# Performance work log

Measured on AMD Instinct MI355X. Metric: run time of the kernel, lower is better.

## Reference

```python
import jax, jax.numpy as jnp
import numpy as np

B, N, D = 8, 1024, 512
H, DH = 8, 64          # num_heads, dim_head_output
MLP = 2048
PRUNE_NUM = 64         # remove_num > 0 -> prune branch of determine_fuse
KEEP_NUM = 3
NEG = -1e10


def setup_inputs() -> dict:
    key = jax.random.key(0)
    ks = jax.random.split(key, 10)
    s = 0.02
    inp = {
        "x": jax.random.normal(ks[0], (B, N, D), dtype=jnp.float32),
        "mask": (jax.random.uniform(ks[1], (B, N, N)) < 0.1).astype(jnp.float32),
        "Wqkv": jax.random.normal(ks[2], (D, 3 * H * DH), dtype=jnp.float32) * s,
        "Wout": jax.random.normal(ks[3], (H * DH, D), dtype=jnp.float32) * s,
        "bout": jnp.zeros((D,), jnp.float32),
        "ln1_g": jnp.ones((D,), jnp.float32),
        "ln1_b": jnp.zeros((D,), jnp.float32),
        "ln2_g": jnp.ones((D,), jnp.float32),
        "ln2_b": jnp.zeros((D,), jnp.float32),
        "W1": jax.random.normal(ks[4], (D, MLP), dtype=jnp.float32) * s,
        "b1": jnp.zeros((MLP,), jnp.float32),
        "W2": jax.random.normal(ks[5], (MLP, D), dtype=jnp.float32) * s,
        "b2": jnp.zeros((D,), jnp.float32),
    }
    return inp


def _layer_norm(x, g, b, eps=1e-5):
    mu = jnp.mean(x, axis=-1, keepdims=True)
    var = jnp.mean((x - mu) ** 2, axis=-1, keepdims=True)
    return (x - mu) * jax.lax.rsqrt(var + eps) * g + b


def _attention_with_gos(h, mask, Wqkv, Wout, bout):
    # qkv projection (no bias), chunk into q,k,v then b n (h d) -> b h n d
    qkv = h @ Wqkv                                  # [B,N,3*H*DH]
    q, k, v = jnp.split(qkv, 3, axis=-1)
    def heads(t):
        return t.reshape(B, N, H, DH).transpose(0, 2, 1, 3)  # bhnd
    q, k, v = heads(q), heads(k), heads(v)
    scale = DH ** -0.5
    scores = jnp.einsum("bhnd,bhmd->bhnm", q, k) * scale
    scores = jnp.where(mask[:, None, :, :] == 1.0, NEG, scores)
    attw = jax.nn.softmax(scores, axis=-1)          # [B,H,N,N]
    out = jnp.einsum("bhnm,bhmd->bhnd", attw, v)
    out = out.transpose(0, 2, 1, 3).reshape(B, N, H * DH)
    out = out @ Wout + bout                         # [B,N,D] (dropout=0 -> identity)

    # att_weights_topk = attw.mean(heads)[:, 0]; [:,0] = -inf
    att_topk = attw.mean(axis=1)[:, 0]              # [B,N]
    att_topk = att_topk.at[:, 0].set(-jnp.inf)

    # determine_fuse (prune branch, remove_num > 0)
    nrm = jnp.linalg.norm(out, axis=2, keepdims=True)
    normed = out / jnp.maximum(nrm, 1e-12)          # F.normalize(p=2, dim=2)
    cos = jnp.einsum("bnd,bmd->bnm", normed, normed)
    idx = jnp.arange(N)
    cos = cos.at[:, idx, idx].set(-jnp.inf)
    cos = cos.at[:, 0, :].set(-jnp.inf)
    cos = cos.at[:, :, 0].set(-jnp.inf)
    # NOTE: torch also computes topk of cos.view(B,-1) with k=(N-1)^2, but the
    # result is unused in the remove_num>0 branch (dead code under jit).

    # torch.topk(att_topk, N) sorted descending -> argsort of -att_topk
    attentive_idx = jnp.argsort(-att_topk, axis=1)  # [B,N]
    # pruned = attentive_idx[:, :N-1][:, -PRUNE_NUM:]
    what_to_prune = attentive_idx[:, N - 1 - PRUNE_NUM : N - 1]
    what_to_merge = jnp.full((B, 1), -1, dtype=jnp.int32)
    survived_mask = jnp.zeros((B, 1 + KEEP_NUM, 1 + KEEP_NUM), dtype=jnp.int32)
    return out, what_to_prune, what_to_merge, survived_mask


def reference(x, mask, Wqkv, Wout, bout, ln1_g, ln1_b, ln2_g, ln2_b, W1, b1, W2, b2):
    h = _layer_norm(x, ln1_g, ln1_b)
    att_out, what_to_prune, what_to_merge, survived_mask = _attention_with_gos(
        h, mask, Wqkv, Wout, bout)
    x = x + att_out
    h2 = _layer_norm(x, ln2_g, ln2_b)
    ff = jax.nn.gelu(h2 @ W1 + b1, approximate=False) @ W2 + b2
    x = x + ff
    return x, what_to_prune, what_to_merge, survived_mask
```

## Files before the change

kernel.cpp:

```cpp
#include <hip/hip_runtime.h>
#include <hip/hip_bf16.h>
#include <math.h>

#define BB 8
#define NN 1024
#define DD 512
#define HH 8
#define DHH 64
#define MLPD 2048

typedef __attribute__((ext_vector_type(8))) short short8;
typedef __attribute__((ext_vector_type(4))) float f32x4;

#define MFMA16(a,b,c) __builtin_amdgcn_mfma_f32_16x16x32_bf16(a,b,c,0,0,0)

#define QSCALE 0.18033688011112042f
#define NEGBIG 0xCE6E6B28u

__device__ __forceinline__ short f2bf(float f) {
  union { float f; unsigned u; } x; x.f = f;
  unsigned r = x.u + 0x7FFFu + ((x.u >> 16) & 1u);
  return (short)(r >> 16);
}

__device__ __forceinline__ void gl_lds16(const short* g, short* l) {
  __builtin_amdgcn_global_load_lds(
      (const __attribute__((address_space(1))) unsigned int*)g,
      (__attribute__((address_space(3))) unsigned int*)l, 16, 0, 0);
}

__device__ __forceinline__ float gelu_fast(float t) {
  const float u = 0.7978845608028654f * (t + 0.044715f * t * t * t);
  const float e = __builtin_amdgcn_exp2f(u * 2.8853900817779268f);
  return t - t * __builtin_amdgcn_rcpf(e + 1.0f);
}

template<bool WF32>
__global__ __launch_bounds__(256) void ln_kernel(const float* __restrict__ x,
    const float* __restrict__ gam, const float* __restrict__ bet,
    short* __restrict__ ob, float* __restrict__ of)
{
  const int row = blockIdx.x;
  const int tid = threadIdx.x;
  const float2 xv = *(const float2*)(x + (size_t)row*DD + tid*2);
  double s = (double)xv.x + (double)xv.y;
  for (int o = 32; o >= 1; o >>= 1) s += __shfl_down(s, o, 64);
  __shared__ double red[4];
  const int l = tid & 63, w = tid >> 6;
  if (l == 0) red[w] = s;
  __syncthreads();
  const double mu = (red[0]+red[1]+red[2]+red[3]) * (1.0/512.0);
  const double d0 = (double)xv.x - mu, d1 = (double)xv.y - mu;
  double q = d0*d0 + d1*d1;
  for (int o = 32; o >= 1; o >>= 1) q += __shfl_down(q, o, 64);
  __syncthreads();
  if (l == 0) red[w] = q;
  __syncthreads();
  const double var = (red[0]+red[1]+red[2]+red[3]) * (1.0/512.0);
  const float rs = (float)(1.0 / sqrt(var + 1e-5));
  const float mf = (float)mu;
  const float y0 = (xv.x - mf)*rs*gam[tid*2]   + bet[tid*2];
  const float y1 = (xv.y - mf)*rs*gam[tid*2+1] + bet[tid*2+1];
  ob[(size_t)row*DD + tid*2]   = f2bf(y0);
  ob[(size_t)row*DD + tid*2+1] = f2bf(y1);
  if (WF32) {
    of[(size_t)row*DD + tid*2]   = y0;
    of[(size_t)row*DD + tid*2+1] = y1;
  }
}

__global__ __launch_bounds__(256) void wtall_kernel(
    const float* __restrict__ Wqkv, const float* __restrict__ Wout,
    const float* __restrict__ W1,   const float* __restrict__ W2,
    short* __restrict__ Wqkvt, short* __restrict__ Woutt,
    short* __restrict__ W1t,   short* __restrict__ W2t)
{
  const int id = blockIdx.x;
  const float* W; short* Wt; int K, N, t;
  if (id < 768)       { W = Wqkv; Wt = Wqkvt; K = 512;  N = 1536; t = id; }
  else if (id < 1024) { W = Wout; Wt = Woutt; K = 512;  N = 512;  t = id - 768; }
  else if (id < 2048) { W = W1;   Wt = W1t;   K = 512;  N = 2048; t = id - 1024; }
  else                { W = W2;   Wt = W2t;   K = 2048; N = 512;  t = id - 2048; }
  const int nx = N >> 5;
  const int n0 = (t % nx)*32, k0 = (t / nx)*32;
  __shared__ float tile[32][33];
  const int tx = threadIdx.x & 31, ty = threadIdx.x >> 5;
  #pragma unroll
  for (int j = 0; j < 4; j++)
    tile[ty + j*8][tx] = W[(size_t)(k0 + ty + j*8)*N + n0 + tx];
  __syncthreads();
  #pragma unroll
  for (int j = 0; j < 4; j++)
    Wt[(size_t)(n0 + ty + j*8)*K + k0 + tx] = f2bf(tile[tx][ty + j*8]);
}

__global__ __launch_bounds__(256) void maskpack_kernel(const float* __restrict__ mask,
    unsigned long long* __restrict__ mb)
{
  const int wid = blockIdx.x*256 + threadIdx.x;
  if (wid >= BB*NN*16) return;
  const int r = wid >> 4, c = wid & 15;
  const float4* p = (const float4*)(mask + (size_t)r*NN + c*64);
  unsigned long long m = 0;
  #pragma unroll
  for (int i = 0; i < 16; i++) {
    const float4 v = p[i];
    unsigned long long mm = 0;
    if (v.x == 1.0f) mm |= 1ULL;
    if (v.y == 1.0f) mm |= 2ULL;
    if (v.z == 1.0f) mm |= 4ULL;
    if (v.w == 1.0f) mm |= 8ULL;
    m |= mm << (i*4);
  }
  mb[wid] = m;
}

template<int BN, int EPI, int NBUF>
__global__ __launch_bounds__(256) void gemm_bt(
    const short* __restrict__ A, const short* __restrict__ Bt,
    int M, int N, int K,
    const float* __restrict__ bias, const float* __restrict__ res,
    float* __restrict__ outf, short* __restrict__ outb,
    short* __restrict__ outQ, short* __restrict__ outK, short* __restrict__ outVt)
{
  constexpr int CH = 8 + BN/16;
  constexpr int L  = CH/4;
  constexpr int BUFS = (128 + BN)*32;
  __shared__ __align__(16) short lds[NBUF*BUFS];
  const int tid = threadIdx.x;
  const int bm0 = blockIdx.x * 128;
  const int bn0 = blockIdx.y * BN;
  const int lane = tid & 63, wid = tid >> 6;
  const int wm = (wid >> 1) * 64, wn = (wid & 1) * (BN/2);
  const int lr = lane & 15, lg = lane >> 4;
  constexpr int NT = BN/32;

  const short* gsrc[L];
  int loff[L];
  const int scc = (((lane & 3) ^ ((lane >> 3) & 3)))*8;
  #pragma unroll
  for (int i = 0; i < L; i++) {
    const int c = i*4 + wid;
    const int rr = ((c < 8) ? c : c - 8)*16 + (lane >> 2);
    gsrc[i] = (c < 8) ? (A + (size_t)(bm0 + rr)*K + scc)
                      : (Bt + (size_t)(bn0 + rr)*K + scc);
    loff[i] = c*512;
  }
  const int xs = (lr >> 1) & 3;

  f32x4 acc[4][NT];
  #pragma unroll
  for (int i = 0; i < 4; i++)
    #pragma unroll
    for (int j = 0; j < NT; j++) acc[i][j] = f32x4{0.f,0.f,0.f,0.f};

  const int nsteps = K >> 5;

  auto STAGE = [&](int buf, int t) {
    short* dst = lds + buf*BUFS;
    const int ko = t*32;
    #pragma unroll
    for (int i = 0; i < L; i++)
      gl_lds16(gsrc[i] + ko, dst + loff[i]);
  };
  auto COMPUTE = [&](const short* bufA) {
    const short* bufB = bufA + 4096;
    short8 af[4], bfr[NT];
    #pragma unroll
    for (int mt = 0; mt < 4; mt++)
      af[mt] = *(const short8*)(bufA + (wm + mt*16 + lr)*32 + (lg ^ xs)*8);
    #pragma unroll
    for (int nt = 0; nt < NT; nt++)
      bfr[nt] = *(const short8*)(bufB + (wn + nt*16 + lr)*32 + (lg ^ xs)*8);
    __builtin_amdgcn_s_setprio(1);
    #pragma unroll
    for (int mt = 0; mt < 4; mt++)
      #pragma unroll
      for (int nt = 0; nt < NT; nt++)
        acc[mt][nt] = MFMA16(af[mt], bfr[nt], acc[mt][nt]);
    __builtin_amdgcn_s_setprio(0);
  };

  if constexpr (NBUF == 2) {
    STAGE(0, 0);
    asm volatile("s_waitcnt vmcnt(0)" ::: "memory");
    __builtin_amdgcn_s_barrier();
    int cur = 0;
    #pragma unroll 1
    for (int t = 0; t < nsteps; t++) {
      if (t + 1 < nsteps) STAGE(cur ^ 1, t + 1);
      COMPUTE(lds + cur*BUFS);
      asm volatile("s_waitcnt vmcnt(0)" ::: "memory");
      __builtin_amdgcn_s_barrier();
      cur ^= 1;
    }
  } else {
    STAGE(0, 0);
    STAGE(1, 1);
    int cur = 0;
    #pragma unroll 1
    for (int t = 0; t < nsteps; t++) {
      if (t == nsteps - 1) {
        asm volatile("s_waitcnt vmcnt(0)" ::: "memory");
      } else if constexpr (L == 4) {
        asm volatile("s_waitcnt vmcnt(4)" ::: "memory");
      } else {
        asm volatile("s_waitcnt vmcnt(3)" ::: "memory");
      }
      __builtin_amdgcn_s_barrier();
      if (t + 2 < nsteps) {
        const int bnext = (cur == 0) ? 2 : cur - 1;
        STAGE(bnext, t + 2);
      }
      COMPUTE(lds + cur*BUFS);
      cur = (cur == 2) ? 0 : cur + 1;
    }
  }

  if (EPI == 0 && bn0 >= 1024) {
    #pragma unroll
    for (int mt = 0; mt < 4; mt++)
      #pragma unroll
      for (int nt = 0; nt < NT; nt++) {
        const int row0 = bm0 + wm + mt*16 + lg*4;
        const int b = row0 >> 10, tok0 = row0 & 1023;
        const int c2 = bn0 + wn + nt*16 + lr - 1024;
        const int h = c2 >> 6, d = c2 & 63;
        unsigned lo2, hi2;
        asm("v_cvt_pk_bf16_f32 %0, %1, %2" : "=v"(lo2)
            : "v"(acc[mt][nt][0]), "v"(acc[mt][nt][1]));
        asm("v_cvt_pk_bf16_f32 %0, %1, %2" : "=v"(hi2)
            : "v"(acc[mt][nt][2]), "v"(acc[mt][nt][3]));
        uint2 pw; pw.x = lo2; pw.y = hi2;
        *(uint2*)(outVt + (((size_t)(b*HH + h))*DHH + d)*NN + tok0) = pw;
      }
    return;
  }

  #pragma unroll
  for (int mt = 0; mt < 4; mt++)
    #pragma unroll
    for (int nt = 0; nt < NT; nt++)
      #pragma unroll
      for (int r = 0; r < 4; r++) {
        const int row = bm0 + wm + mt*16 + lg*4 + r;
        const int col = bn0 + wn + nt*16 + lr;
        const float v = acc[mt][nt][r];
        if (EPI == 0) {
          const int b = row >> 10, tok = row & 1023;
          if (col < 512) {
            const int h = col >> 6, d = col & 63;
            outQ[(((size_t)(b*HH + h))*NN + tok)*DHH + d] = f2bf(v * QSCALE);
          } else {
            const int c2 = col - 512, h = c2 >> 6, d = c2 & 63;
            outK[(((size_t)(b*HH + h))*NN + tok)*DHH + d] = f2bf(v);
          }
        } else if (EPI == 1) {
          outf[(size_t)row*N + col] = v + bias[col] + res[(size_t)row*N + col];
        } else {
          outb[(size_t)row*N + col] = f2bf(gelu_fast(v + bias[col]));
        }
      }
}

__global__ __launch_bounds__(256) void attn_kernel(
    const short* __restrict__ Qg, const short* __restrict__ Kg,
    const short* __restrict__ Vtg, const unsigned long long* __restrict__ mb,
    short* __restrict__ attout)
{
  const int id = blockIdx.x;
  const int bh = (id & 7)*8 + ((id >> 3) & 7);
  const int qb = id >> 6;
  const int b = bh >> 3, h = bh & 7;
  const int tid = threadIdx.x, lane = tid & 63, w = tid >> 6;
  const int lr = lane & 15, lg = lane >> 4;

  __shared__ __align__(16) short K0[64*64], K1[64*64];
  __shared__ __align__(16) short V0[64*64], V1[64*64];
  __shared__ __align__(16) short PsA[4][16*72], PsB[4][16*72];

  const int qA = qb*128 + w*32 + lr;
  const int qB = qA + 16;
  short* PsAw = &PsA[w][0];
  short* PsBw = &PsB[w][0];

  const size_t qbase = (size_t)bh*NN*DHH;
  const short8 bqA0 = *(const short8*)(Qg + qbase + (size_t)qA*DHH + lg*8);
  const short8 bqA1 = *(const short8*)(Qg + qbase + (size_t)qA*DHH + 32 + lg*8);
  const short8 bqB0 = *(const short8*)(Qg + qbase + (size_t)qB*DHH + lg*8);
  const short8 bqB1 = *(const short8*)(Qg + qbase + (size_t)qB*DHH + 32 + lg*8);

  const unsigned long long* mrowA = mb + ((size_t)b*NN + qA)*16;
  const unsigned long long* mrowB = mb + ((size_t)b*NN + qB)*16;

  const int l8 = lane >> 3;
  const int uu = (lane & 7) ^ l8;
  const short* kgA = Kg + ((size_t)bh*NN + w*16 + l8)*64 + uu*8;
  const short* kgB = kgA + 8*64;
  const short* vgA = Vtg + ((size_t)bh*DHH + w*16 + l8)*NN + uu*8;
  const short* vgB = vgA + 8*NN;
  auto STAGE = [&](short* kb, short* vb, int kc) {
    gl_lds16(kgA + kc*4096, kb + (w*16)*64);
    gl_lds16(kgB + kc*4096, kb + (w*16 + 8)*64);
    gl_lds16(vgA + kc*64,   vb + (w*16)*64);
    gl_lds16(vgB + kc*64,   vb + (w*16 + 8)*64);
  };
  const int xo0 = ((lg ^ (lr & 7)))*8;
  const int xo1 = (((lg ^ (lr & 7))) ^ 4)*8;

  unsigned long long mAc, mBc, mAn, mBn;

  STAGE(K0, V0, 0);
  mAc = mrowA[0]; mBc = mrowB[0];
  asm volatile("s_waitcnt vmcnt(0)" ::: "memory");
  __builtin_amdgcn_s_barrier();

  f32x4 oA[4], oB[4];
  #pragma unroll
  for (int dt = 0; dt < 4; dt++) { oA[dt] = f32x4{0.f,0.f,0.f,0.f}; oB[dt] = f32x4{0.f,0.f,0.f,0.f}; }
  float lsumA = 0.f, lsumB = 0.f;

#define ATT_BODY(CK, CV, NK, NV, MAc, MBc, MAn, MBn, KC, LAST)                 \
  {                                                                            \
    if (!(LAST)) {                                                             \
      STAGE(NK, NV, (KC)+1);                                                   \
      MAn = mrowA[(KC)+1]; MBn = mrowB[(KC)+1];                                \
    }                                                                          \
                              \
    f32x4 sA[4], sB[4];                                                        \
    {                                                                          \
      const unsigned long long mqA = MAc >> (lg*4);                            \
      const unsigned loA = (unsigned)mqA, hiA = (unsigned)(mqA >> 32);         \
      const unsigned long long mqB = MBc >> (lg*4);                            \
      const unsigned loB = (unsigned)mqB, hiB = (unsigned)(mqB >> 32);         \
      _Pragma("unroll")                                                        \
      for (int nt = 0; nt < 4; nt++) {                                         \
        const unsigned wA = (nt < 2) ? loA : hiA;                              \
        const unsigned wB = (nt < 2) ? loB : hiB;                              \
        const int sh = (nt & 1) * 16;                                          \
        _Pragma("unroll")                                                      \
        for (int rr = 0; rr < 4; rr++) {                                       \
          const unsigned bA = (wA >> (sh + rr)) & 1u;                          \
          const unsigned bB = (wB >> (sh + rr)) & 1u;                          \
          sA[nt][rr] = __uint_as_float((0u - bA) & NEGBIG);                    \
          sB[nt][rr] = __uint_as_float((0u - bB) & NEGBIG);                    \
        }                                                                      \
      }                                                                        \
    }                                                                          \
    __builtin_amdgcn_s_setprio(1);                                             \
    _Pragma("unroll")                                                          \
    for (int nt = 0; nt < 4; nt++) {                                           \
      const short* kr = (CK) + (nt*16 + lr)*64;                                \
      const short8 ak0 = *(const short8*)(kr + xo0);                           \
      const short8 ak1 = *(const short8*)(kr + xo1);                           \
      sA[nt] = MFMA16(ak0, bqA0, sA[nt]);                                      \
      sA[nt] = MFMA16(ak1, bqA1, sA[nt]);                                      \
      sB[nt] = MFMA16(ak0, bqB0, sB[nt]);                                      \
      sB[nt] = MFMA16(ak1, bqB1, sB[nt]);                                      \
    }                                                                          \
    __builtin_amdgcn_s_setprio(0);                                             \
    _Pragma("unroll")                                                          \
    for (int nt = 0; nt < 4; nt++) {                                           \
      const float a0 = __builtin_amdgcn_exp2f(sA[nt][0]);                      \
      const float a1 = __builtin_amdgcn_exp2f(sA[nt][1]);                      \
      const float a2 = __builtin_amdgcn_exp2f(sA[nt][2]);                      \
      const float a3 = __builtin_amdgcn_exp2f(sA[nt][3]);                      \
      lsumA += (a0 + a1) + (a2 + a3);                                          \
      unsigned plo, phi;                                                       \
      asm("v_cvt_pk_bf16_f32 %0, %1, %2" : "=v"(plo) : "v"(a0), "v"(a1));      \
      asm("v_cvt_pk_bf16_f32 %0, %1, %2" : "=v"(phi) : "v"(a2), "v"(a3));      \
      uint2 pw; pw.x = plo; pw.y = phi;                                        \
      *(uint2*)(PsAw + lr*72 + nt*16 + lg*4) = pw;                             \
      const float c0 = __builtin_amdgcn_exp2f(sB[nt][0]);                      \
      const float c1 = __builtin_amdgcn_exp2f(sB[nt][1]);                      \
      const float c2 = __builtin_amdgcn_exp2f(sB[nt][2]);                      \
      const float c3 = __builtin_amdgcn_exp2f(sB[nt][3]);                      \
      lsumB += (c0 + c1) + (c2 + c3);                                          \
      unsigned qlo, qhi;                                                       \
      asm("v_cvt_pk_bf16_f32 %0, %1, %2" : "=v"(qlo) : "v"(c0), "v"(c1));      \
      asm("v_cvt_pk_bf16_f32 %0, %1, %2" : "=v"(qhi) : "v"(c2), "v"(c3));      \
      uint2 qw; qw.x = qlo; qw.y = qhi;                                        \
      *(uint2*)(PsBw + lr*72 + nt*16 + lg*4) = qw;                             \
    }                                                                          \
    {                                                                          \
      const short8 bpA0 = *(const short8*)(PsAw + lr*72 + lg*8);               \
      const short8 bpA1 = *(const short8*)(PsAw + lr*72 + 32 + lg*8);          \
      const short8 bpB0 = *(const short8*)(PsBw + lr*72 + lg*8);               \
      const short8 bpB1 = *(const short8*)(PsBw + lr*72 + 32 + lg*8);          \
      __builtin_amdgcn_s_setprio(1);                                           \
      _Pragma("unroll")                                                        \
      for (int dt = 0; dt < 4; dt++) {                                         \
        const short* vr = (CV) + (dt*16 + lr)*64;                              \
        const short8 av0 = *(const short8*)(vr + xo0);                         \
        const short8 av1 = *(const short8*)(vr + xo1);                         \
        oA[dt] = MFMA16(av0, bpA0, oA[dt]);                                    \
        oA[dt] = MFMA16(av1, bpA1, oA[dt]);                                    \
        oB[dt] = MFMA16(av0, bpB0, oB[dt]);                                    \
        oB[dt] = MFMA16(av1, bpB1, oB[dt]);                                    \
      }                                                                        \
      __builtin_amdgcn_s_setprio(0);                                           \
    }                                                                          \
    if (!(LAST)) {                                                             \
      asm volatile("s_waitcnt vmcnt(0)" ::: "memory");                         \
      __builtin_amdgcn_s_barrier();                                            \
      MAc = MAn; MBc = MBn;                                                    \
    }                                                                          \
  }

  #pragma unroll 1
  for (int kc = 0; kc < 16; kc += 2) {
    ATT_BODY(K0, V0, K1, V1, mAc, mBc, mAn, mBn, kc, false)
    ATT_BODY(K1, V1, K0, V0, mAc, mBc, mAn, mBn, kc+1, (kc+1) == 15)
  }
#undef ATT_BODY

  lsumA += __shfl_xor(lsumA, 16, 64);
  lsumA += __shfl_xor(lsumA, 32, 64);
  lsumB += __shfl_xor(lsumB, 16, 64);
  lsumB += __shfl_xor(lsumB, 32, 64);
  const float linvA = 1.0f / lsumA;
  const float linvB = 1.0f / lsumB;

  #pragma unroll
  for (int dt = 0; dt < 4; dt++) {
    unsigned w0, w1, w2, w3;
    const float a0 = oA[dt][0]*linvA, a1 = oA[dt][1]*linvA;
    const float a2 = oA[dt][2]*linvA, a3 = oA[dt][3]*linvA;
    asm("v_cvt_pk_bf16_f32 %0, %1, %2" : "=v"(w0) : "v"(a0), "v"(a1));
    asm("v_cvt_pk_bf16_f32 %0, %1, %2" : "=v"(w1) : "v"(a2), "v"(a3));
    uint2 ow; ow.x = w0; ow.y = w1;
    *(uint2*)(PsAw + lr*72 + dt*16 + lg*4) = ow;
    const float c0 = oB[dt][0]*linvB, c1 = oB[dt][1]*linvB;
    const float c2 = oB[dt][2]*linvB, c3 = oB[dt][3]*linvB;
    asm("v_cvt_pk_bf16_f32 %0, %1, %2" : "=v"(w2) : "v"(c0), "v"(c1));
    asm("v_cvt_pk_bf16_f32 %0, %1, %2" : "=v"(w3) : "v"(c2), "v"(c3));
    uint2 ow2; ow2.x = w2; ow2.y = w3;
    *(uint2*)(PsBw + lr*72 + dt*16 + lg*4) = ow2;
  }
  #pragma unroll
  for (int rep = 0; rep < 2; rep++) {
    const int c = lane + rep*64;
    const int row = c >> 3, off = c & 7;
    const uint4 ovA = *(const uint4*)(PsAw + row*72 + off*8);
    *(uint4*)(attout + ((size_t)b*NN + qb*128 + w*32 + row)*DD + h*DHH + off*8) = ovA;
    const uint4 ovB = *(const uint4*)(PsBw + row*72 + off*8);
    *(uint4*)(attout + ((size_t)b*NN + qb*128 + w*32 + 16 + row)*DD + h*DHH + off*8) = ovB;
  }
}

__global__ __launch_bounds__(512) void q0wv_kernel(const float* __restrict__ hlnf,
    const float* __restrict__ Wqkv, double* __restrict__ wv)
{
  const int bh = blockIdx.x, b = bh >> 3, h = bh & 7;
  __shared__ double red[512];
  __shared__ double q0s[64];
  {
    const int d = threadIdx.x & 63, cg = threadIdx.x >> 6;
    double acc = 0.0;
    #pragma unroll 8
    for (int c = cg*64; c < cg*64 + 64; c++)
      acc += (double)hlnf[(size_t)b*NN*DD + c] * (double)Wqkv[(size_t)c*1536 + h*64 + d];
    red[threadIdx.x] = acc;
    __syncthreads();
    if (threadIdx.x < 64) {
      double s = 0.0;
      #pragma unroll
      for (int g = 0; g < 8; g++) s += red[g*64 + d];
      q0s[d] = s;
    }
    __syncthreads();
  }
  const int c = threadIdx.x;
  const float4* wp = (const float4*)(Wqkv + (size_t)c*1536 + 512 + h*64);
  double acc = 0.0;
  #pragma unroll
  for (int dv = 0; dv < 16; dv++) {
    const float4 wq = wp[dv];
    acc += q0s[dv*4+0]*(double)wq.x + q0s[dv*4+1]*(double)wq.y
         + q0s[dv*4+2]*(double)wq.z + q0s[dv*4+3]*(double)wq.w;
  }
  wv[(size_t)bh*512 + c] = acc;
}

__global__ __launch_bounds__(256) void srow_kernel(const float* __restrict__ hlnf,
    const double* __restrict__ wv, const float* __restrict__ mask,
    double* __restrict__ srow)
{
  const int b = blockIdx.x, jc = blockIdx.y;
  const int jl = threadIdx.x >> 3;
  const int cg = threadIdx.x & 7;
  const int j  = jc*32 + jl;
  __shared__ double lw[8*512];
  __shared__ double red[32][8][9];
  for (int i = threadIdx.x; i < 4096; i += 256) lw[i] = wv[(size_t)b*4096 + i];
  __syncthreads();
  double acc[8] = {0,0,0,0,0,0,0,0};
  const float* xr = hlnf + ((size_t)b*NN + j)*DD;
  #pragma unroll
  for (int i = 0; i < 16; i++) {
    const int c = cg*4 + i*32;
    const float4 xv4 = *(const float4*)(xr + c);
    #pragma unroll
    for (int h = 0; h < 8; h++) {
      const double* lwc = lw + h*512 + c;
      acc[h] += (double)xv4.x*lwc[0] + (double)xv4.y*lwc[1]
              + (double)xv4.z*lwc[2] + (double)xv4.w*lwc[3];
    }
  }
  #pragma unroll
  for (int h = 0; h < 8; h++) red[jl][cg][h] = acc[h];
  __syncthreads();
  const int j2 = threadIdx.x >> 3, h2 = threadIdx.x & 7;
  double s = 0.0;
  #pragma unroll
  for (int g = 0; g < 8; g++) s += red[j2][g][h2];
  s *= 0.125;
  const float mval = mask[(size_t)b*NN*NN + jc*32 + j2];
  if (mval == 1.0f) s = -1e10;
  srow[((size_t)b*8 + h2)*NN + jc*32 + j2] = s;
}

__global__ __launch_bounds__(1024) void sumatt_kernel(const double* __restrict__ srow,
    double* __restrict__ attv)
{
  const int b = blockIdx.x;
  const int t = threadIdx.x;
  __shared__ double e[8][1024];
  __shared__ double red[1024];
  __shared__ double sinv[8];
  const int h = t >> 7, j0 = t & 127;
  double ps = 0.0;
  #pragma unroll
  for (int i = 0; i < 8; i++) {
    const int j = j0 + i*128;
    const double v = exp(srow[((size_t)b*8 + h)*NN + j]);
    e[h][j] = v;
    ps += v;
  }
  red[t] = ps;
  __syncthreads();
  #pragma unroll
  for (int off = 64; off >= 1; off >>= 1) {
    if (j0 < off) red[t] += red[t + off];
    __syncthreads();
  }
  if (j0 == 0) sinv[h] = 1.0 / red[t];
  __syncthreads();
  double s = 0.0;
  #pragma unroll
  for (int hh = 0; hh < 8; hh++) s += e[hh][t] * sinv[hh];
  attv[b*NN + t] = (t == 0) ? -INFINITY : s * 0.125;
}

__global__ __launch_bounds__(256) void rank_kernel(const double* __restrict__ attv,
    float* __restrict__ dout, int offP, int offM, int offS)
{
  const int b = blockIdx.x, jc = blockIdx.y;
  const int t = threadIdx.x;
  __shared__ double a[1024];
  __shared__ int red[32][8];
  #pragma unroll
  for (int rep = 0; rep < 4; rep++)
    a[rep*256 + t] = attv[b*NN + rep*256 + t];
  __syncthreads();
  const int jl = t >> 3, kg = t & 7;
  const int j = jc*32 + jl;
  const double aj = a[j];
  int r = 0;
  #pragma unroll 8
  for (int i = 0; i < 128; i++) {
    const int idx = kg*128 + ((i + kg*2) & 127);
    const double ak = a[idx];
    r += ((ak > aj) || (ak == aj && idx < j)) ? 1 : 0;
  }
  red[jl][kg] = r;
  __syncthreads();
  if (t < 32) {
    int rr = 0;
    #pragma unroll
    for (int g = 0; g < 8; g++) rr += red[t][g];
    const int jj = jc*32 + t;
    if (rr >= 959 && rr <= 1022) dout[offP + b*64 + (rr - 959)] = (float)jj;
  }
  if (b == 0 && jc == 0) {
    if (t < 8)   dout[offM + t] = -1.0f;
    if (t < 128) dout[offS + t] = 0.0f;
  }
}

extern "C" void kernel_launch(void* const* d_in, const int* in_sizes, int n_in,
                              void* d_out, int out_size, void* d_ws, size_t ws_size,
                              hipStream_t stream) {
  (void)in_sizes; (void)n_in; (void)out_size; (void)ws_size;
  const float* x     = (const float*)d_in[0];
  const float* mask  = (const float*)d_in[1];
  const float* Wqkv  = (const float*)d_in[2];
  const float* Wout  = (const float*)d_in[3];
  const float* bout  = (const float*)d_in[4];
  const float* ln1g  = (const float*)d_in[5];
  const float* ln1b  = (const float*)d_in[6];
  const float* ln2g  = (const float*)d_in[7];
  const float* ln2b  = (const float*)d_in[8];
  const float* W1    = (const float*)d_in[9];
  const float* b1    = (const float*)d_in[10];
  const float* W2    = (const float*)d_in[11];
  const float* b2    = (const float*)d_in[12];
  float* dout = (float*)d_out;

  const size_t MB = 1ull << 20;
  char* ws = (char*)d_ws;
  short*  hln_bf = (short*)(ws + 0);
  float*  hlnf   = (float*)(ws + 8*MB);
  short*  Qg     = (short*)(ws + 24*MB);
  short*  Kg     = (short*)(ws + 32*MB);
  short*  Vtg    = (short*)(ws + 40*MB);
  unsigned long long* mbits = (unsigned long long*)(ws + 48*MB);
  short*  Wqkvt  = (short*)(ws + 49*MB);
  short*  Woutt  = (short*)(ws + 51*MB);
  short*  W1t    = (short*)(ws + 52*MB);
  short*  W2t    = (short*)(ws + 54*MB);
  double* wvv    = (double*)(ws + 56*MB + 256*1024);
  double* srow   = (double*)(ws + 57*MB);
  double* attv   = (double*)(ws + 59*MB);
  short*  attout = (short*)(ws + 60*MB);
  float*  x1     = (float*)(ws + 68*MB);
  short*  h2     = (short*)(ws + 84*MB);
  short*  gbuf   = (short*)(ws + 0);

  const int offP = BB*NN*DD;
  const int offM = offP + BB*64;
  const int offS = offM + BB;

  ln_kernel<true><<<BB*NN, 256, 0, stream>>>(x, ln1g, ln1b, hln_bf, hlnf);

  q0wv_kernel<<<BB*HH, 512, 0, stream>>>(hlnf, Wqkv, wvv);
  srow_kernel<<<dim3(BB, 32), 256, 0, stream>>>(hlnf, wvv, mask, srow);
  sumatt_kernel<<<BB, 1024, 0, stream>>>(srow, attv);
  rank_kernel<<<dim3(BB, 32), 256, 0, stream>>>(attv, dout, offP, offM, offS);

  maskpack_kernel<<<(BB*NN*16)/256, 256, 0, stream>>>(mask, mbits);
  wtall_kernel<<<3072, 256, 0, stream>>>(Wqkv, Wout, W1, W2,
      Wqkvt, Woutt, W1t, W2t);

  gemm_bt<128,0,3><<<dim3(64, 12), 256, 0, stream>>>(hln_bf, Wqkvt, BB*NN, 1536, 512,
      nullptr, nullptr, nullptr, nullptr, Qg, Kg, Vtg);

  attn_kernel<<<512, 256, 0, stream>>>(Qg, Kg, Vtg, mbits, attout);

  gemm_bt<64,1,3><<<dim3(64, 8), 256, 0, stream>>>(attout, Woutt, BB*NN, 512, 512,
      bout, x, x1, nullptr, nullptr, nullptr, nullptr);

  ln_kernel<false><<<BB*NN, 256, 0, stream>>>(x1, ln2g, ln2b, h2, nullptr);

  gemm_bt<64,2,3><<<dim3(64, 32), 256, 0, stream>>>(h2, W1t, BB*NN, 2048, 512,
      b1, nullptr, nullptr, gbuf, nullptr, nullptr, nullptr);

  gemm_bt<64,1,3><<<dim3(64, 8), 256, 0, stream>>>(gbuf, W2t, BB*NN, 512, 2048,
      b2, x1, dout, nullptr, nullptr, nullptr, nullptr);
}
```

Before: 196.4 us.

## Fuse prep kernels, store residual in bf16, widen FFN1 GEMM tile

Merges the first layer norm, mask bit-packing and weight transpose/convert into a single prep kernel to cut launch count. The post-attention residual is stored as bf16 instead of fp32, with a new epilogue mode that writes bf16 and another that reads the bf16 residual for the final add. The second layer norm reads this bf16 buffer. The FFN1 GEMM switches to a 128-wide N tile with double buffering. The bf16 residual reduces memory traffic but loses precision in the skip connection.

Measured after the change: 189.1 us. 3.7% less time.

```diff
diff --git a/kernel.cpp b/kernel.cpp
--- a/kernel.cpp
+++ b/kernel.cpp
@@ -22,6 +22,11 @@
   unsigned r = x.u + 0x7FFFu + ((x.u >> 16) & 1u);
   return (short)(r >> 16);
 }
+__device__ __forceinline__ float bf2f(short s) {
+  union { float f; unsigned u; } x;
+  x.u = ((unsigned)(unsigned short)s) << 16;
+  return x.f;
+}
 
 __device__ __forceinline__ void gl_lds16(const short* g, short* l) {
   __builtin_amdgcn_global_load_lds(
@@ -35,22 +40,96 @@
   return t - t * __builtin_amdgcn_rcpf(e + 1.0f);
 }
 
-template<bool WF32>
-__global__ __launch_bounds__(256) void ln_kernel(const float* __restrict__ x,
+__global__ __launch_bounds__(256) void prep_kernel(
+    const float* __restrict__ x, const float* __restrict__ ln1g,
+    const float* __restrict__ ln1b, short* __restrict__ hln_bf,
+    float* __restrict__ hlnf,
+    const float* __restrict__ mask, unsigned long long* __restrict__ mbits,
+    const float* __restrict__ Wqkv, const float* __restrict__ Wout,
+    const float* __restrict__ W1,   const float* __restrict__ W2,
+    short* __restrict__ Wqkvt, short* __restrict__ Woutt,
+    short* __restrict__ W1t,   short* __restrict__ W2t)
+{
+  const int id = blockIdx.x;
+  const int tid = threadIdx.x;
+  if (id < 8192) {
+    __shared__ double red[4];
+    const int row = id;
+    const float2 xv = *(const float2*)(x + (size_t)row*DD + tid*2);
+    double s = (double)xv.x + (double)xv.y;
+    for (int o = 32; o >= 1; o >>= 1) s += __shfl_down(s, o, 64);
+    const int l = tid & 63, w = tid >> 6;
+    if (l == 0) red[w] = s;
+    __syncthreads();
+    const double mu = (red[0]+red[1]+red[2]+red[3]) * (1.0/512.0);
+    const double d0 = (double)xv.x - mu, d1 = (double)xv.y - mu;
+    double q = d0*d0 + d1*d1;
+    for (int o = 32; o >= 1; o >>= 1) q += __shfl_down(q, o, 64);
+    __syncthreads();
+    if (l == 0) red[w] = q;
+    __syncthreads();
+    const double var = (red[0]+red[1]+red[2]+red[3]) * (1.0/512.0);
+    const float rs = (float)(1.0 / sqrt(var + 1e-5));
+    const float mf = (float)mu;
+    const float y0 = (xv.x - mf)*rs*ln1g[tid*2]   + ln1b[tid*2];
+    const float y1 = (xv.y - mf)*rs*ln1g[tid*2+1] + ln1b[tid*2+1];
+    hln_bf[(size_t)row*DD + tid*2]   = f2bf(y0);
+    hln_bf[(size_t)row*DD + tid*2+1] = f2bf(y1);
+    hlnf[(size_t)row*DD + tid*2]   = y0;
+    hlnf[(size_t)row*DD + tid*2+1] = y1;
+  } else if (id < 8704) {
+    const int wid = (id - 8192)*256 + tid;
+    const int r = wid >> 4, c = wid & 15;
+    const float4* p = (const float4*)(mask + (size_t)r*NN + c*64);
+    unsigned long long m = 0;
+    #pragma unroll
+    for (int i = 0; i < 16; i++) {
+      const float4 v = p[i];
+      unsigned long long mm = 0;
+      if (v.x == 1.0f) mm |= 1ULL;
+      if (v.y == 1.0f) mm |= 2ULL;
+      if (v.z == 1.0f) mm |= 4ULL;
+      if (v.w == 1.0f) mm |= 8ULL;
+      m |= mm << (i*4);
+    }
+    mbits[wid] = m;
+  } else {
+    const int id2 = id - 8704;
+    const float* W; short* Wt; int K, N, t;
+    if (id2 < 768)       { W = Wqkv; Wt = Wqkvt; K = 512;  N = 1536; t = id2; }
+    else if (id2 < 1024) { W = Wout; Wt = Woutt; K = 512;  N = 512;  t = id2 - 768; }
+    else if (id2 < 2048) { W = W1;   Wt = W1t;   K = 512;  N = 2048; t = id2 - 1024; }
+    else                 { W = W2;   Wt = W2t;   K = 2048; N = 512;  t = id2 - 2048; }
+    const int nx = N >> 5;
+    const int n0 = (t % nx)*32, k0 = (t / nx)*32;
+    __shared__ float tile[32][33];
+    const int tx = tid & 31, ty = tid >> 5;
+    #pragma unroll
+    for (int j = 0; j < 4; j++)
+      tile[ty + j*8][tx] = W[(size_t)(k0 + ty + j*8)*N + n0 + tx];
+    __syncthreads();
+    #pragma unroll
+    for (int j = 0; j < 4; j++)
+      Wt[(size_t)(n0 + ty + j*8)*K + k0 + tx] = f2bf(tile[tx][ty + j*8]);
+  }
+}
+
+__global__ __launch_bounds__(256) void ln2_kernel(const short* __restrict__ xb,
     const float* __restrict__ gam, const float* __restrict__ bet,
-    short* __restrict__ ob, float* __restrict__ of)
+    short* __restrict__ ob)
 {
   const int row = blockIdx.x;
   const int tid = threadIdx.x;
-  const float2 xv = *(const float2*)(x + (size_t)row*DD + tid*2);
-  double s = (double)xv.x + (double)xv.y;
+  const short2 xs = *(const short2*)(xb + (size_t)row*DD + tid*2);
+  const float x0 = bf2f(xs.x), x1v = bf2f(xs.y);
+  double s = (double)x0 + (double)x1v;
   for (int o = 32; o >= 1; o >>= 1) s += __shfl_down(s, o, 64);
   __shared__ double red[4];
   const int l = tid & 63, w = tid >> 6;
   if (l == 0) red[w] = s;
   __syncthreads();
   const double mu = (red[0]+red[1]+red[2]+red[3]) * (1.0/512.0);
-  const double d0 = (double)xv.x - mu, d1 = (double)xv.y - mu;
+  const double d0 = (double)x0 - mu, d1 = (double)x1v - mu;
   double q = d0*d0 + d1*d1;
   for (int o = 32; o >= 1; o >>= 1) q += __shfl_down(q, o, 64);
   __syncthreads();
@@ -59,60 +138,8 @@
   const double var = (red[0]+red[1]+red[2]+red[3]) * (1.0/512.0);
   const float rs = (float)(1.0 / sqrt(var + 1e-5));
   const float mf = (float)mu;
-  const float y0 = (xv.x - mf)*rs*gam[tid*2]   + bet[tid*2];
-  const float y1 = (xv.y - mf)*rs*gam[tid*2+1] + bet[tid*2+1];
-  ob[(size_t)row*DD + tid*2]   = f2bf(y0);
-  ob[(size_t)row*DD + tid*2+1] = f2bf(y1);
-  if (WF32) {
-    of[(size_t)row*DD + tid*2]   = y0;
-    of[(size_t)row*DD + tid*2+1] = y1;
-  }
-}
-
-__global__ __launch_bounds__(256) void wtall_kernel(
-    const float* __restrict__ Wqkv, const float* __restrict__ Wout,
-    const float* __restrict__ W1,   const float* __restrict__ W2,
-    short* __restrict__ Wqkvt, short* __restrict__ Woutt,
-    short* __restrict__ W1t,   short* __restrict__ W2t)
-{
-  const int id = blockIdx.x;
-  const float* W; short* Wt; int K, N, t;
-  if (id < 768)       { W = Wqkv; Wt = Wqkvt; K = 512;  N = 1536; t = id; }
-  else if (id < 1024) { W = Wout; Wt = Woutt; K = 512;  N = 512;  t = id - 768; }
-  else if (id < 2048) { W = W1;   Wt = W1t;   K = 512;  N = 2048; t = id - 1024; }
-  else                { W = W2;   Wt = W2t;   K = 2048; N = 512;  t = id - 2048; }
-  const int nx = N >> 5;
-  const int n0 = (t % nx)*32, k0 = (t / nx)*32;
-  __shared__ float tile[32][33];
-  const int tx = threadIdx.x & 31, ty = threadIdx.x >> 5;
-  #pragma unroll
-  for (int j = 0; j < 4; j++)
-    tile[ty + j*8][tx] = W[(size_t)(k0 + ty + j*8)*N + n0 + tx];
-  __syncthreads();
-  #pragma unroll
-  for (int j = 0; j < 4; j++)
-    Wt[(size_t)(n0 + ty + j*8)*K + k0 + tx] = f2bf(tile[tx][ty + j*8]);
-}
-
-__global__ __launch_bounds__(256) void maskpack_kernel(const float* __restrict__ mask,
-    unsigned long long* __restrict__ mb)
-{
-  const int wid = blockIdx.x*256 + threadIdx.x;
-  if (wid >= BB*NN*16) return;
-  const int r = wid >> 4, c = wid & 15;
-  const float4* p = (const float4*)(mask + (size_t)r*NN + c*64);
-  unsigned long long m = 0;
-  #pragma unroll
-  for (int i = 0; i < 16; i++) {
-    const float4 v = p[i];
-    unsigned long long mm = 0;
-    if (v.x == 1.0f) mm |= 1ULL;
-    if (v.y == 1.0f) mm |= 2ULL;
-    if (v.z == 1.0f) mm |= 4ULL;
-    if (v.w == 1.0f) mm |= 8ULL;
-    m |= mm << (i*4);
-  }
-  mb[wid] = m;
+  ob[(size_t)row*DD + tid*2]   = f2bf((x0  - mf)*rs*gam[tid*2]   + bet[tid*2]);
+  ob[(size_t)row*DD + tid*2+1] = f2bf((x1v - mf)*rs*gam[tid*2+1] + bet[tid*2+1]);
 }
 
 template<int BN, int EPI, int NBUF>
@@ -120,6 +147,7 @@
     const short* __restrict__ A, const short* __restrict__ Bt,
     int M, int N, int K,
     const float* __restrict__ bias, const float* __restrict__ res,
+    const short* __restrict__ resb,
     float* __restrict__ outf, short* __restrict__ outb,
     short* __restrict__ outQ, short* __restrict__ outK, short* __restrict__ outVt)
 {
@@ -255,10 +283,12 @@
             const int c2 = col - 512, h = c2 >> 6, d = c2 & 63;
             outK[(((size_t)(b*HH + h))*NN + tok)*DHH + d] = f2bf(v);
           }
-        } else if (EPI == 1) {
-          outf[(size_t)row*N + col] = v + bias[col] + res[(size_t)row*N + col];
+        } else if (EPI == 2) {
+          outb[(size_t)row*N + col] = f2bf(gelu_fast(v + bias[col]));
+        } else if (EPI == 3) {
+          outb[(size_t)row*N + col] = f2bf(v + bias[col] + res[(size_t)row*N + col]);
         } else {
-          outb[(size_t)row*N + col] = f2bf(gelu_fast(v + bias[col]));
+          outf[(size_t)row*N + col] = v + bias[col] + bf2f(resb[(size_t)row*N + col]);
         }
       }
 }
@@ -326,7 +356,6 @@
       STAGE(NK, NV, (KC)+1);                                                   \
       MAn = mrowA[(KC)+1]; MBn = mrowB[(KC)+1];                                \
     }                                                                          \
-                              \
     f32x4 sA[4], sB[4];                                                        \
     {                                                                          \
       const unsigned long long mqA = MAc >> (lg*4);                            \
@@ -623,7 +652,7 @@
   double* srow   = (double*)(ws + 57*MB);
   double* attv   = (double*)(ws + 59*MB);
   short*  attout = (short*)(ws + 60*MB);
-  float*  x1     = (float*)(ws + 68*MB);
+  short*  x1b    = (short*)(ws + 68*MB);
   short*  h2     = (short*)(ws + 84*MB);
   short*  gbuf   = (short*)(ws + 0);
 
@@ -631,30 +660,27 @@
   const int offM = offP + BB*64;
   const int offS = offM + BB;
 
-  ln_kernel<true><<<BB*NN, 256, 0, stream>>>(x, ln1g, ln1b, hln_bf, hlnf);
+  prep_kernel<<<11776, 256, 0, stream>>>(x, ln1g, ln1b, hln_bf, hlnf,
+      mask, mbits, Wqkv, Wout, W1, W2, Wqkvt, Woutt, W1t, W2t);
 
   q0wv_kernel<<<BB*HH, 512, 0, stream>>>(hlnf, Wqkv, wvv);
   srow_kernel<<<dim3(BB, 32), 256, 0, stream>>>(hlnf, wvv, mask, srow);
   sumatt_kernel<<<BB, 1024, 0, stream>>>(srow, attv);
   rank_kernel<<<dim3(BB, 32), 256, 0, stream>>>(attv, dout, offP, offM, offS);
 
-  maskpack_kernel<<<(BB*NN*16)/256, 256, 0, stream>>>(mask, mbits);
-  wtall_kernel<<<3072, 256, 0, stream>>>(Wqkv, Wout, W1, W2,
-      Wqkvt, Woutt, W1t, W2t);
-
   gemm_bt<128,0,3><<<dim3(64, 12), 256, 0, stream>>>(hln_bf, Wqkvt, BB*NN, 1536, 512,
-      nullptr, nullptr, nullptr, nullptr, Qg, Kg, Vtg);
+      nullptr, nullptr, nullptr, nullptr, nullptr, Qg, Kg, Vtg);
 
   attn_kernel<<<512, 256, 0, stream>>>(Qg, Kg, Vtg, mbits, attout);
 
-  gemm_bt<64,1,3><<<dim3(64, 8), 256, 0, stream>>>(attout, Woutt, BB*NN, 512, 512,
-      bout, x, x1, nullptr, nullptr, nullptr, nullptr);
-
-  ln_kernel<false><<<BB*NN, 256, 0, stream>>>(x1, ln2g, ln2b, h2, nullptr);
-
-  gemm_bt<64,2,3><<<dim3(64, 32), 256, 0, stream>>>(h2, W1t, BB*NN, 2048, 512,
-      b1, nullptr, nullptr, gbuf, nullptr, nullptr, nullptr);
-
-  gemm_bt<64,1,3><<<dim3(64, 8), 256, 0, stream>>>(gbuf, W2t, BB*NN, 512, 2048,
-      b2, x1, dout, nullptr, nullptr, nullptr, nullptr);
-}
+  gemm_bt<64,3,3><<<dim3(64, 8), 256, 0, stream>>>(attout, Woutt, BB*NN, 512, 512,
+      bout, x, nullptr, nullptr, x1b, nullptr, nullptr, nullptr);
+
+  ln2_kernel<<<BB*NN, 256, 0, stream>>>(x1b, ln2g, ln2b, h2);
+
+  gemm_bt<128,2,2><<<dim3(64, 16), 256, 0, stream>>>(h2, W1t, BB*NN, 2048, 512,
+      b1, nullptr, nullptr, nullptr, gbuf, nullptr, nullptr, nullptr);
+
+  gemm_bt<64,4,3><<<dim3(64, 8), 256, 0, stream>>>(gbuf, W2t, BB*NN, 512, 2048,
+      b2, nullptr, x1b, dout, nullptr, nullptr, nullptr, nullptr);
+}
```
